# Performance work log

Hardware: AMD Instinct MI355X
Metric: run time of the kernel (lower is better)

The kernel has to match this reference:

```python
import jax, jax.numpy as jnp
import numpy as np

N_NODES = 100000
N_EDGES = 1000000
D = 64
N_LAYERS = 3
LN_EPS = 1e-5


def setup_inputs() -> dict:
    key = jax.random.key(0)
    ks = jax.random.split(key, 12)
    s = 1.0 / np.sqrt(D)
    return {
        "feats": jax.random.normal(ks[0], (N_NODES, D), jnp.float32),
        "src": jax.random.randint(ks[1], (N_EDGES,), 0, N_NODES, jnp.int32),
        "dst": jax.random.randint(ks[2], (N_EDGES,), 0, N_NODES, jnp.int32),
        # GraphConv weights/biases (stacked over layers; in==hid==out==D)
        "conv_W": jax.random.normal(ks[3], (N_LAYERS, D, D), jnp.float32) * s,
        "conv_b": jnp.zeros((N_LAYERS, D), jnp.float32),
        # residual Linear per layer
        "res_W": jax.random.normal(ks[4], (N_LAYERS, D, D), jnp.float32) * s,
        "res_b": jnp.zeros((N_LAYERS, D), jnp.float32),
        # LayerNorm affine per layer
        "ln_g": jnp.ones((N_LAYERS, D), jnp.float32),
        "ln_b": jnp.zeros((N_LAYERS, D), jnp.float32),
        # final linear_prediction
        "pred_W": jax.random.normal(ks[5], (D, D), jnp.float32) * s,
        "pred_b": jnp.zeros((D,), jnp.float32),
    }


def _layer_norm(h, g, b):
    mu = jnp.mean(h, axis=-1, keepdims=True)
    var = jnp.mean(jnp.square(h - mu), axis=-1, keepdims=True)
    return (h - mu) * jax.lax.rsqrt(var + LN_EPS) * g + b


def reference(feats, src, dst, conv_W, conv_b, res_W, res_b, ln_g, ln_b, pred_W, pred_b):
    n = feats.shape[0]
    ones = jnp.ones(src.shape[0], feats.dtype)
    # DGL GraphConv norm='both', degrees clamped to >= 1
    out_deg = jnp.clip(jax.ops.segment_sum(ones, src, num_segments=n), 1.0, None)
    in_deg = jnp.clip(jax.ops.segment_sum(ones, dst, num_segments=n), 1.0, None)
    out_norm = jax.lax.rsqrt(out_deg)[:, None]  # [N,1]
    in_norm = jax.lax.rsqrt(in_deg)[:, None]

    h = feats
    h_final = jnp.zeros_like(feats)
    for i in range(N_LAYERS):
        # GraphConv: scale src, sum-aggregate over edges, scale dst, linear
        msg = (h * out_norm)[src]                                   # [E, D]
        agg = jax.ops.segment_sum(msg, dst, num_segments=n) * in_norm
        conv = agg @ conv_W[i] + conv_b[i]
        # residual linear + LayerNorm + relu (dropout p=0) + JK accumulate
        h = conv + h @ res_W[i] + res_b[i]
        h = jax.nn.relu(_layer_norm(h, ln_g[i], ln_b[i]))
        h_final = h_final + h
    return h_final @ pred_W + pred_b
```

## Files before the change

### kernel.cpp

```cpp
#include <hip/hip_runtime.h>
#include <hip/hip_bf16.h>

#define DD 64
#define NBLK 128
#define MAXBUK 1024
#define BSHIFT 7

typedef __attribute__((ext_vector_type(8))) short short8v;
typedef __attribute__((ext_vector_type(4))) float f32x4;

__device__ __forceinline__ unsigned pk_bf16(float a, float b) {
    __hip_bfloat162 h = __float22bfloat162_rn(make_float2(a, b));
    unsigned u; __builtin_memcpy(&u, &h, 4); return u;
}
__device__ __forceinline__ short f2bf_s(float f) {
    union { float f; unsigned u; } x; x.f = f;
    unsigned r = x.u + 0x7fff + ((x.u >> 16) & 1);
    return (short)(r >> 16);
}
__device__ __forceinline__ float bf_lo(unsigned u) { return __int_as_float(u << 16); }
__device__ __forceinline__ float bf_hi(unsigned u) { return __int_as_float(u & 0xffff0000u); }
__device__ __forceinline__ short8v u4_to_s8(uint4 u) {
    union { uint4 u; short8v s; } x; x.u = u; return x.s;
}


__global__ __launch_bounds__(256) void part_count(
        const int* __restrict__ src, const int* __restrict__ dst,
        int* __restrict__ cnt, int E, int nbuk, int ce) {
    __shared__ int hd[MAXBUK], hs[MAXBUK];
    for (int i = threadIdx.x; i < MAXBUK; i += 256) { hd[i] = 0; hs[i] = 0; }
    __syncthreads();
    int e0 = blockIdx.x * ce;
    int e1 = min(e0 + ce, E);
    for (int e = e0 + (int)threadIdx.x; e < e1; e += 256) {
        atomicAdd(&hd[dst[e] >> BSHIFT], 1);
        atomicAdd(&hs[src[e] >> BSHIFT], 1);
    }
    __syncthreads();
    int L2 = nbuk * NBLK;
    for (int b = threadIdx.x; b < nbuk; b += 256) {
        cnt[b * NBLK + blockIdx.x]      = hd[b];
        cnt[L2 + b * NBLK + blockIdx.x] = hs[b];
    }
}

__global__ void scan1p(int* __restrict__ a, int* __restrict__ bsums, int L) {
    __shared__ int tmp[256];
    int gid = blockIdx.x * 256 + threadIdx.x;
    int v = (gid < L) ? a[gid] : 0;
    tmp[threadIdx.x] = v;
    __syncthreads();
    for (int off = 1; off < 256; off <<= 1) {
        int t = (threadIdx.x >= off) ? tmp[threadIdx.x - off] : 0;
        __syncthreads();
        tmp[threadIdx.x] += t;
        __syncthreads();
    }
    if (gid < L) a[gid] = tmp[threadIdx.x] - v;
    if (threadIdx.x == 255) bsums[blockIdx.x] = tmp[255];
}
__global__ void scan2p(int* __restrict__ bsums, int nb) {
    __shared__ int tmp[1024];
    int v = (threadIdx.x < (unsigned)nb) ? bsums[threadIdx.x] : 0;
    tmp[threadIdx.x] = v;
    __syncthreads();
    for (int off = 1; off < 1024; off <<= 1) {
        int t = (threadIdx.x >= off) ? tmp[threadIdx.x - off] : 0;
        __syncthreads();
        tmp[threadIdx.x] += t;
        __syncthreads();
    }
    if (threadIdx.x < (unsigned)nb) bsums[threadIdx.x] = tmp[threadIdx.x] - v;
}
__global__ void scan3p(int* __restrict__ a, const int* __restrict__ bsums, int L) {
    int gid = blockIdx.x * 256 + threadIdx.x;
    if (gid < L) a[gid] += bsums[blockIdx.x];
}

__global__ __launch_bounds__(256) void part_scatter(
        const int* __restrict__ src, const int* __restrict__ dst,
        const int* __restrict__ ofs,
        unsigned int* __restrict__ partD, unsigned char* __restrict__ partS,
        int E, int nbuk, int ce) {
    __shared__ int cd[MAXBUK], cs[MAXBUK];
    int L2 = nbuk * NBLK;
    for (int b = threadIdx.x; b < nbuk; b += 256) {
        cd[b] = ofs[b * NBLK + blockIdx.x];
        cs[b] = ofs[L2 + b * NBLK + blockIdx.x] - E;
    }
    __syncthreads();
    int e0 = blockIdx.x * ce;
    int e1 = min(e0 + ce, E);
    for (int e = e0 + (int)threadIdx.x; e < e1; e += 256) {
        int s = src[e], d = dst[e];
        int pd = atomicAdd(&cd[d >> BSHIFT], 1);
        partD[pd] = ((unsigned)(d & 127) << 17) | (unsigned)s;
        int ps = atomicAdd(&cs[s >> BSHIFT], 1);
        partS[ps] = (unsigned char)(s & 127);
    }
}

__global__ __launch_bounds__(256) void bucket_csr(
        const unsigned int* __restrict__ partD, const int* __restrict__ ofs,
        int* __restrict__ rowptr, int* __restrict__ esrc,
        float* __restrict__ inn, int E, int nbuk, int n) {
    __shared__ int h[128], sc[128], cu[128];
    int b = blockIdx.x, tid = threadIdx.x;
    int e0 = ofs[b * NBLK];
    int e1 = (b + 1 < nbuk) ? ofs[(b + 1) * NBLK] : E;
    if (tid < 128) h[tid] = 0;
    __syncthreads();
    for (int e = e0 + tid; e < e1; e += 256)
        atomicAdd(&h[partD[e] >> 17], 1);
    __syncthreads();
    if (tid < 128) sc[tid] = h[tid];
    __syncthreads();
    for (int off = 1; off < 128; off <<= 1) {
        int t = (tid < 128 && tid >= off) ? sc[tid - off] : 0;
        __syncthreads();
        if (tid < 128) sc[tid] += t;
        __syncthreads();
    }
    int nodeBase = b << BSHIFT;
    if (tid < 128) {
        int excl = e0 + sc[tid] - h[tid];
        cu[tid] = excl;
        int v = nodeBase + tid;
        if (v < n) {
            rowptr[v] = excl;
            inn[v] = rsqrtf((float)max(h[tid], 1));
        }
    }
    if (b == 0 && tid == 0) rowptr[n] = E;
    __syncthreads();
    for (int e = e0 + tid; e < e1; e += 256) {
        unsigned v = partD[e];
        int p = atomicAdd(&cu[v >> 17], 1);
        esrc[p] = (int)(v & 0x1FFFFu);
    }
}

__global__ __launch_bounds__(256) void bucket_deg(
        const unsigned char* __restrict__ partS, const int* __restrict__ ofs,
        float* __restrict__ outn, float* __restrict__ rs,
        int E, int nbuk, int n) {
    __shared__ int h[128];
    int b = blockIdx.x, tid = threadIdx.x;
    int L2 = nbuk * NBLK;
    int f0 = ofs[L2 + b * NBLK] - E;
    int f1 = (b + 1 < nbuk) ? ofs[L2 + (b + 1) * NBLK] - E : E;
    if (tid < 128) h[tid] = 0;
    __syncthreads();
    for (int e = f0 + tid; e < f1; e += 256)
        atomicAdd(&h[(int)partS[e]], 1);
    __syncthreads();
    if (tid < 128) {
        int v = (b << BSHIFT) + tid;
        if (v < n) {
            float d = (float)max(h[tid], 1);
            outn[v] = rsqrtf(d);
            rs[v]   = sqrtf(d);
        }
    }
}

__global__ void scale_kernel(const float* __restrict__ feats, const float* __restrict__ outn,
                             unsigned short* __restrict__ hs, int n) {
    int idx = blockIdx.x * blockDim.x + threadIdx.x;
    if (idx < n * 8) {
        int v = idx >> 3;
        float s = outn[v];
        const float4* fp = (const float4*)feats + (size_t)idx * 2;
        float4 f0 = fp[0], f1 = fp[1];
        uint4 o;
        o.x = pk_bf16(f0.x * s, f0.y * s); o.y = pk_bf16(f0.z * s, f0.w * s);
        o.z = pk_bf16(f1.x * s, f1.y * s); o.w = pk_bf16(f1.z * s, f1.w * s);
        ((uint4*)hs)[idx] = o;
    }
}

__global__ __launch_bounds__(256) void gcn_kernel(
    const int* __restrict__ rowptr, const int* __restrict__ esrc,
    const float* __restrict__ inn, const float* __restrict__ rs,
    const float* __restrict__ outn,
    const unsigned short* __restrict__ hs_in,
    const float* __restrict__ Wc, const float* __restrict__ bc,
    const float* __restrict__ Wr, const float* __restrict__ br,
    const float* __restrict__ Wp, const float* __restrict__ pb,
    const float* __restrict__ g, const float* __restrict__ bb,
    unsigned short* __restrict__ hs_out, float* __restrict__ h_final,
    float* __restrict__ pred_out,
    int first, int last, int n)
{
    __shared__ __align__(16) short sWf[24 * 64 * 8];
    __shared__ __align__(16) short sXa[4][16 * 72];
    __shared__ float sEps[4 * 64];

    int lane = threadIdx.x & 63;
    int wave = threadIdx.x >> 6;
    int q   = lane & 15;
    int gg  = lane >> 4;
    int q8  = lane & 7;
    int o8  = lane >> 3;

    for (int idx = threadIdx.x; idx < 64; idx += blockDim.x) {
        sEps[idx]       = bc[idx] + br[idx];
        sEps[64 + idx]  = g[idx];
        sEps[128 + idx] = bb[idx];
        sEps[192 + idx] = pb[idx];
    }
    for (int f = wave * 6; f < wave * 6 + 6; ++f) {
        int mat = f >> 3, ft = (f >> 1) & 3, kc = f & 1;
        const float* Ws = (mat == 0) ? Wc : (mat == 1) ? Wr : Wp;
        int feat = ft * 16 + q;
        int k0 = kc * 32 + gg * 8;
        short8v fr;
        #pragma unroll
        for (int j = 0; j < 8; ++j) fr[j] = f2bf_s(Ws[(k0 + j) * DD + feat]);
        *(short8v*)&sWf[(f * 64 + lane) * 8] = fr;
    }
    __syncthreads();

    short* xrow_w = &sXa[wave][0];
    const short8v* wf = (const short8v*)sWf;
    int wgid = blockIdx.x * 4 + wave;
    int nwav = gridDim.x * 4;
    int ngrp = (n + 15) >> 4;

    for (int grp = wgid; grp < ngrp; grp += nwav) {
        int vbase = grp << 4;
        int vo = vbase + q;
        int vsel = min(vo, n - 1);

        const uint4* hrow = (const uint4*)(hs_in + (size_t)vsel * DD);
        uint4 bh0u = hrow[gg];
        uint4 bh1u = hrow[4 + gg];
        float rsv  = rs[vsel];
        float innv = inn[vsel];

        int rp = rowptr[min(vbase + min(lane, 16), n)];
        int stA = __shfl(rp, o8);     int dgA = __shfl(rp, o8 + 1) - stA;
        int stB = __shfl(rp, o8 + 8); int dgB = __shfl(rp, o8 + 9) - stB;

        #pragma unroll
        for (int hh = 0; hh < 2; ++hh) {
            int st = hh ? stB : stA;
            int dg = hh ? dgB : dgA;
            int mdg = dg;
            mdg = max(mdg, __shfl_xor(mdg, 8));
            mdg = max(mdg, __shfl_xor(mdg, 16));
            mdg = max(mdg, __shfl_xor(mdg, 32));

            float a[8];
            #pragma unroll
            for (int c = 0; c < 8; ++c) a[c] = 0.0f;

            int id0 = (0 < dg) ? esrc[st + 0] : 0;  float m0 = (0 < dg) ? 1.f : 0.f;
            int id1 = (1 < dg) ? esrc[st + 1] : 0;  float m1 = (1 < dg) ? 1.f : 0.f;
            int id2 = (2 < dg) ? esrc[st + 2] : 0;  float m2 = (2 < dg) ? 1.f : 0.f;
            int id3 = (3 < dg) ? esrc[st + 3] : 0;  float m3 = (3 < dg) ? 1.f : 0.f;

            for (int t = 0; t < mdg; t += 4) {
                uint4 r0 = *(const uint4*)(hs_in + (size_t)id0 * DD + q8 * 8);
                uint4 r1 = *(const uint4*)(hs_in + (size_t)id1 * DD + q8 * 8);
                uint4 r2 = *(const uint4*)(hs_in + (size_t)id2 * DD + q8 * 8);
                uint4 r3 = *(const uint4*)(hs_in + (size_t)id3 * DD + q8 * 8);
                float c0 = m0, c1 = m1, c2 = m2, c3 = m3;
                int t4 = t + 4;
                id0 = (t4 + 0 < dg) ? esrc[st + t4 + 0] : 0;  m0 = (t4 + 0 < dg) ? 1.f : 0.f;
                id1 = (t4 + 1 < dg) ? esrc[st + t4 + 1] : 0;  m1 = (t4 + 1 < dg) ? 1.f : 0.f;
                id2 = (t4 + 2 < dg) ? esrc[st + t4 + 2] : 0;  m2 = (t4 + 2 < dg) ? 1.f : 0.f;
                id3 = (t4 + 3 < dg) ? esrc[st + t4 + 3] : 0;  m3 = (t4 + 3 < dg) ? 1.f : 0.f;
                a[0] = fmaf(bf_lo(r0.x), c0, a[0]); a[1] = fmaf(bf_hi(r0.x), c0, a[1]);
                a[2] = fmaf(bf_lo(r0.y), c0, a[2]); a[3] = fmaf(bf_hi(r0.y), c0, a[3]);
                a[4] = fmaf(bf_lo(r0.z), c0, a[4]); a[5] = fmaf(bf_hi(r0.z), c0, a[5]);
                a[6] = fmaf(bf_lo(r0.w), c0, a[6]); a[7] = fmaf(bf_hi(r0.w), c0, a[7]);
                a[0] = fmaf(bf_lo(r1.x), c1, a[0]); a[1] = fmaf(bf_hi(r1.x), c1, a[1]);
                a[2] = fmaf(bf_lo(r1.y), c1, a[2]); a[3] = fmaf(bf_hi(r1.y), c1, a[3]);
                a[4] = fmaf(bf_lo(r1.z), c1, a[4]); a[5] = fmaf(bf_hi(r1.z), c1, a[5]);
                a[6] = fmaf(bf_lo(r1.w), c1, a[6]); a[7] = fmaf(bf_hi(r1.w), c1, a[7]);
                a[0] = fmaf(bf_lo(r2.x), c2, a[0]); a[1] = fmaf(bf_hi(r2.x), c2, a[1]);
                a[2] = fmaf(bf_lo(r2.y), c2, a[2]); a[3] = fmaf(bf_hi(r2.y), c2, a[3]);
                a[4] = fmaf(bf_lo(r2.z), c2, a[4]); a[5] = fmaf(bf_hi(r2.z), c2, a[5]);
                a[6] = fmaf(bf_lo(r2.w), c2, a[6]); a[7] = fmaf(bf_hi(r2.w), c2, a[7]);
                a[0] = fmaf(bf_lo(r3.x), c3, a[0]); a[1] = fmaf(bf_hi(r3.x), c3, a[1]);
                a[2] = fmaf(bf_lo(r3.y), c3, a[2]); a[3] = fmaf(bf_hi(r3.y), c3, a[3]);
                a[4] = fmaf(bf_lo(r3.z), c3, a[4]); a[5] = fmaf(bf_hi(r3.z), c3, a[5]);
                a[6] = fmaf(bf_lo(r3.w), c3, a[6]); a[7] = fmaf(bf_hi(r3.w), c3, a[7]);
            }

            uint4 w4;
            w4.x = pk_bf16(a[0], a[1]); w4.y = pk_bf16(a[2], a[3]);
            w4.z = pk_bf16(a[4], a[5]); w4.w = pk_bf16(a[6], a[7]);
            *(uint4*)&xrow_w[(hh * 8 + o8) * 72 + q8 * 8] = w4;
        }

        const short* xr = &xrow_w[q * 72];
        short8v ba0 = *(const short8v*)&xr[gg * 8];
        short8v ba1 = *(const short8v*)&xr[32 + gg * 8];
        short8v sh0 = u4_to_s8(bh0u);
        short8v sh1 = u4_to_s8(bh1u);

        f32x4 accC[4], accR[4];
        #pragma unroll
        for (int ft = 0; ft < 4; ++ft) {
            f32x4 c = {0.f, 0.f, 0.f, 0.f};
            c = __builtin_amdgcn_mfma_f32_16x16x32_bf16(wf[(ft * 2 + 0) * 64 + lane], ba0, c, 0, 0, 0);
            c = __builtin_amdgcn_mfma_f32_16x16x32_bf16(wf[(ft * 2 + 1) * 64 + lane], ba1, c, 0, 0, 0);
            accC[ft] = c;
            f32x4 r = {0.f, 0.f, 0.f, 0.f};
            r = __builtin_amdgcn_mfma_f32_16x16x32_bf16(wf[(8 + ft * 2 + 0) * 64 + lane], sh0, r, 0, 0, 0);
            r = __builtin_amdgcn_mfma_f32_16x16x32_bf16(wf[(8 + ft * 2 + 1) * 64 + lane], sh1, r, 0, 0, 0);
            accR[ft] = r;
        }

        f32x4 ac[4];
        #pragma unroll
        for (int ft = 0; ft < 4; ++ft) {
            float4 b4 = *(const float4*)&sEps[ft * 16 + gg * 4];
            ac[ft][0] = fmaf(innv, accC[ft][0], fmaf(rsv, accR[ft][0], b4.x));
            ac[ft][1] = fmaf(innv, accC[ft][1], fmaf(rsv, accR[ft][1], b4.y));
            ac[ft][2] = fmaf(innv, accC[ft][2], fmaf(rsv, accR[ft][2], b4.z));
            ac[ft][3] = fmaf(innv, accC[ft][3], fmaf(rsv, accR[ft][3], b4.w));
        }
        float s = 0.f;
        #pragma unroll
        for (int ft = 0; ft < 4; ++ft) s += ac[ft][0] + ac[ft][1] + ac[ft][2] + ac[ft][3];
        s += __shfl_xor(s, 16); s += __shfl_xor(s, 32);
        float mu = s * (1.0f / 64.0f);
        float vsum = 0.f;
        #pragma unroll
        for (int ft = 0; ft < 4; ++ft) {
            #pragma unroll
            for (int r = 0; r < 4; ++r) { float d = ac[ft][r] - mu; vsum += d * d; }
        }
        vsum += __shfl_xor(vsum, 16); vsum += __shfl_xor(vsum, 32);
        float rinv = rsqrtf(vsum * (1.0f / 64.0f) + 1e-5f);

        float4 yv[4];
        #pragma unroll
        for (int ft = 0; ft < 4; ++ft) {
            float4 g4 = *(const float4*)&sEps[64 + ft * 16 + gg * 4];
            float4 c4 = *(const float4*)&sEps[128 + ft * 16 + gg * 4];
            yv[ft].x = fmaxf((ac[ft][0] - mu) * rinv * g4.x + c4.x, 0.f);
            yv[ft].y = fmaxf((ac[ft][1] - mu) * rinv * g4.y + c4.y, 0.f);
            yv[ft].z = fmaxf((ac[ft][2] - mu) * rinv * g4.z + c4.z, 0.f);
            yv[ft].w = fmaxf((ac[ft][3] - mu) * rinv * g4.w + c4.w, 0.f);
        }

        if (!last) {
            if (vo < n) {
                float on = outn[vo];
                #pragma unroll
                for (int ft = 0; ft < 4; ++ft) {
                    size_t off = (size_t)vo * DD + ft * 16 + gg * 4;
                    uint2 p;
                    p.x = pk_bf16(yv[ft].x * on, yv[ft].y * on);
                    p.y = pk_bf16(yv[ft].z * on, yv[ft].w * on);
                    *(uint2*)&hs_out[off] = p;
                    if (first) {
                        *(float4*)&h_final[off] = yv[ft];
                    } else {
                        float4 hf = *(const float4*)&h_final[off];
                        hf.x += yv[ft].x; hf.y += yv[ft].y;
                        hf.z += yv[ft].z; hf.w += yv[ft].w;
                        *(float4*)&h_final[off] = hf;
                    }
                }
            }
        } else {
            #pragma unroll
            for (int ft = 0; ft < 4; ++ft) {
                float4 hf = make_float4(0.f, 0.f, 0.f, 0.f);
                if (vo < n) {
                    float4 old = *(const float4*)&h_final[(size_t)vo * DD + ft * 16 + gg * 4];
                    hf.x = old.x + yv[ft].x; hf.y = old.y + yv[ft].y;
                    hf.z = old.z + yv[ft].z; hf.w = old.w + yv[ft].w;
                }
                uint2 p;
                p.x = pk_bf16(hf.x, hf.y);
                p.y = pk_bf16(hf.z, hf.w);
                *(uint2*)&xrow_w[q * 72 + ft * 16 + gg * 4] = p;
            }
            short8v bp0 = *(const short8v*)&xr[gg * 8];
            short8v bp1 = *(const short8v*)&xr[32 + gg * 8];
            #pragma unroll
            for (int ft = 0; ft < 4; ++ft) {
                f32x4 p = {0.f, 0.f, 0.f, 0.f};
                p = __builtin_amdgcn_mfma_f32_16x16x32_bf16(wf[(16 + ft * 2 + 0) * 64 + lane], bp0, p, 0, 0, 0);
                p = __builtin_amdgcn_mfma_f32_16x16x32_bf16(wf[(16 + ft * 2 + 1) * 64 + lane], bp1, p, 0, 0, 0);
                if (vo < n) {
                    float4 b4 = *(const float4*)&sEps[192 + ft * 16 + gg * 4];
                    float4 o = make_float4(p[0] + b4.x, p[1] + b4.y, p[2] + b4.z, p[3] + b4.w);
                    *(float4*)&pred_out[(size_t)vo * DD + ft * 16 + gg * 4] = o;
                }
            }
        }
    }
}

extern "C" void kernel_launch(void* const* d_in, const int* in_sizes, int n_in,
                              void* d_out, int out_size, void* d_ws, size_t ws_size,
                              hipStream_t stream) {
    const float* feats  = (const float*)d_in[0];
    const int*   src    = (const int*)d_in[1];
    const int*   dst    = (const int*)d_in[2];
    const float* conv_W = (const float*)d_in[3];
    const float* conv_b = (const float*)d_in[4];
    const float* res_W  = (const float*)d_in[5];
    const float* res_b  = (const float*)d_in[6];
    const float* ln_g   = (const float*)d_in[7];
    const float* ln_b   = (const float*)d_in[8];
    const float* pred_W = (const float*)d_in[9];
    const float* pred_b = (const float*)d_in[10];

    int N = in_sizes[0] / DD;
    int E = in_sizes[1];

    int nbuk = (N + (1 << BSHIFT) - 1) >> BSHIFT;
    int ce   = (E + NBLK - 1) / NBLK;
    int L    = nbuk * NBLK * 2;
    int nb   = (L + 255) / 256;

    int*   rowptr = (int*)d_ws;
    int*   cnt    = rowptr + (N + 1);
    int*   bsums  = cnt + MAXBUK * NBLK * 2;
    int*   esrc   = bsums + 1024;
    float* outn   = (float*)(esrc + E);
    float* inn    = outn + N;
    float* rs     = inn + N;
    float* base   = (float*)(((uintptr_t)(rs + N) + 15) & ~(uintptr_t)15);
    unsigned short* hsA = (unsigned short*)base;
    unsigned short* hsB = (unsigned short*)(base + (size_t)N * 32);
    float* hfin  = base + (size_t)N * 64;
    unsigned int*  partD = (unsigned int*)hfin;
    unsigned char* partS = (unsigned char*)(partD + E);

    part_count  <<<NBLK, 256, 0, stream>>>(src, dst, cnt, E, nbuk, ce);
    scan1p      <<<nb, 256, 0, stream>>>(cnt, bsums, L);
    scan2p      <<<1, 1024, 0, stream>>>(bsums, nb);
    scan3p      <<<nb, 256, 0, stream>>>(cnt, bsums, L);
    part_scatter<<<NBLK, 256, 0, stream>>>(src, dst, cnt, partD, partS, E, nbuk, ce);
    bucket_csr  <<<nbuk, 256, 0, stream>>>(partD, cnt, rowptr, esrc, inn, E, nbuk, N);
    bucket_deg  <<<nbuk, 256, 0, stream>>>(partS, cnt, outn, rs, E, nbuk, N);
    scale_kernel<<<(N * 8 + 255) / 256, 256, 0, stream>>>(feats, outn, hsA, N);

    const unsigned short* ins[3]  = {hsA, hsB, hsA};
    unsigned short*       outs[3] = {hsB, hsA, hsB};
    for (int l = 0; l < 3; ++l) {
        gcn_kernel<<<1024, 256, 0, stream>>>(
            rowptr, esrc, inn, rs, outn, ins[l],
            conv_W + (size_t)l * DD * DD, conv_b + (size_t)l * DD,
            res_W  + (size_t)l * DD * DD, res_b  + (size_t)l * DD,
            pred_W, pred_b,
            ln_g   + (size_t)l * DD,      ln_b   + (size_t)l * DD,
            outs[l], hfin, (float*)d_out,
            (l == 0) ? 1 : 0, (l == 2) ? 1 : 0, N);
    }
}
```

Baseline: 303.5 us.

## Sort nodes by in-degree and process both half-groups in one merged gather loop

Adds a counting sort of destination nodes by in-degree (histogram, scan, scatter kernels) and makes the fused GCN kernel walk nodes in that order, so each 16-node wave group has similar degrees and fewer masked iterations in the gather loop. The two 8-node halves are now gathered together in one loop with twice the outstanding loads, the next group's perm and rowptr entries are prefetched, and the grid drops to 768 blocks with a 3-blocks-per-CU launch bound. The cost is five extra small preprocessing kernels, scattered output writes through the permutation, and higher register pressure.

New measurement: 424.7 us. 39.9% more time.

```diff
diff --git a/kernel.cpp b/kernel.cpp
--- a/kernel.cpp
+++ b/kernel.cpp
@@ -5,6 +5,7 @@
 #define NBLK 128
 #define MAXBUK 1024
 #define BSHIFT 7
+#define NB3 64
 
 typedef __attribute__((ext_vector_type(8))) short short8v;
 typedef __attribute__((ext_vector_type(4))) float f32x4;
@@ -104,7 +105,8 @@
 __global__ __launch_bounds__(256) void bucket_csr(
         const unsigned int* __restrict__ partD, const int* __restrict__ ofs,
         int* __restrict__ rowptr, int* __restrict__ esrc,
-        float* __restrict__ inn, int E, int nbuk, int n) {
+        float* __restrict__ inn, int* __restrict__ degout,
+        int E, int nbuk, int n) {
     __shared__ int h[128], sc[128], cu[128];
     int b = blockIdx.x, tid = threadIdx.x;
     int e0 = ofs[b * NBLK];
@@ -130,6 +132,7 @@
         if (v < n) {
             rowptr[v] = excl;
             inn[v] = rsqrtf((float)max(h[tid], 1));
+            degout[v] = h[tid];
         }
     }
     if (b == 0 && tid == 0) rowptr[n] = E;
@@ -162,6 +165,32 @@
             outn[v] = rsqrtf(d);
             rs[v]   = sqrtf(d);
         }
+    }
+}
+
+__global__ __launch_bounds__(256) void dhist(const int* __restrict__ deg,
+                                             int* __restrict__ cnt2, int N, int chunk) {
+    __shared__ int h2[256];
+    h2[threadIdx.x] = 0;
+    __syncthreads();
+    int b = blockIdx.x;
+    int v0 = b * chunk, v1 = min(v0 + chunk, N);
+    for (int v = v0 + (int)threadIdx.x; v < v1; v += 256)
+        atomicAdd(&h2[min(deg[v], 255)], 1);
+    __syncthreads();
+    cnt2[threadIdx.x * NB3 + b] = h2[threadIdx.x];
+}
+__global__ __launch_bounds__(256) void dscatter(const int* __restrict__ deg,
+                                                const int* __restrict__ cnt2,
+                                                int* __restrict__ perm, int N, int chunk) {
+    __shared__ int cu2[256];
+    int b = blockIdx.x;
+    cu2[threadIdx.x] = cnt2[threadIdx.x * NB3 + b];
+    __syncthreads();
+    int v0 = b * chunk, v1 = min(v0 + chunk, N);
+    for (int v = v0 + (int)threadIdx.x; v < v1; v += 256) {
+        int pos = atomicAdd(&cu2[min(deg[v], 255)], 1);
+        perm[pos] = v;
     }
 }
 
@@ -180,8 +209,9 @@
     }
 }
 
-__global__ __launch_bounds__(256) void gcn_kernel(
+__global__ __launch_bounds__(256, 3) void gcn_kernel(
     const int* __restrict__ rowptr, const int* __restrict__ esrc,
+    const int* __restrict__ perm,
     const float* __restrict__ inn, const float* __restrict__ rs,
     const float* __restrict__ outn,
     const unsigned short* __restrict__ hs_in,
@@ -228,72 +258,116 @@
     int nwav = gridDim.x * 4;
     int ngrp = (n + 15) >> 4;
 
+    int nodeL = 0, rpS = 0, rpE = 0;
+    if (wgid < ngrp && lane < 16) {
+        nodeL = perm[min(wgid * 16 + lane, n - 1)];
+        rpS = rowptr[nodeL];
+        rpE = rowptr[nodeL + 1];
+    }
+
     for (int grp = wgid; grp < ngrp; grp += nwav) {
-        int vbase = grp << 4;
-        int vo = vbase + q;
-        int vsel = min(vo, n - 1);
-
-        const uint4* hrow = (const uint4*)(hs_in + (size_t)vsel * DD);
+        int idxq = (grp << 4) + q;
+        int pv   = __shfl(nodeL, q);
+
+        const uint4* hrow = (const uint4*)(hs_in + (size_t)pv * DD);
         uint4 bh0u = hrow[gg];
         uint4 bh1u = hrow[4 + gg];
-        float rsv  = rs[vsel];
-        float innv = inn[vsel];
-
-        int rp = rowptr[min(vbase + min(lane, 16), n)];
-        int stA = __shfl(rp, o8);     int dgA = __shfl(rp, o8 + 1) - stA;
-        int stB = __shfl(rp, o8 + 8); int dgB = __shfl(rp, o8 + 9) - stB;
-
-        #pragma unroll
-        for (int hh = 0; hh < 2; ++hh) {
-            int st = hh ? stB : stA;
-            int dg = hh ? dgB : dgA;
-            int mdg = dg;
-            mdg = max(mdg, __shfl_xor(mdg, 8));
-            mdg = max(mdg, __shfl_xor(mdg, 16));
-            mdg = max(mdg, __shfl_xor(mdg, 32));
-
-            float a[8];
-            #pragma unroll
-            for (int c = 0; c < 8; ++c) a[c] = 0.0f;
-
-            int id0 = (0 < dg) ? esrc[st + 0] : 0;  float m0 = (0 < dg) ? 1.f : 0.f;
-            int id1 = (1 < dg) ? esrc[st + 1] : 0;  float m1 = (1 < dg) ? 1.f : 0.f;
-            int id2 = (2 < dg) ? esrc[st + 2] : 0;  float m2 = (2 < dg) ? 1.f : 0.f;
-            int id3 = (3 < dg) ? esrc[st + 3] : 0;  float m3 = (3 < dg) ? 1.f : 0.f;
-
-            for (int t = 0; t < mdg; t += 4) {
-                uint4 r0 = *(const uint4*)(hs_in + (size_t)id0 * DD + q8 * 8);
-                uint4 r1 = *(const uint4*)(hs_in + (size_t)id1 * DD + q8 * 8);
-                uint4 r2 = *(const uint4*)(hs_in + (size_t)id2 * DD + q8 * 8);
-                uint4 r3 = *(const uint4*)(hs_in + (size_t)id3 * DD + q8 * 8);
-                float c0 = m0, c1 = m1, c2 = m2, c3 = m3;
-                int t4 = t + 4;
-                id0 = (t4 + 0 < dg) ? esrc[st + t4 + 0] : 0;  m0 = (t4 + 0 < dg) ? 1.f : 0.f;
-                id1 = (t4 + 1 < dg) ? esrc[st + t4 + 1] : 0;  m1 = (t4 + 1 < dg) ? 1.f : 0.f;
-                id2 = (t4 + 2 < dg) ? esrc[st + t4 + 2] : 0;  m2 = (t4 + 2 < dg) ? 1.f : 0.f;
-                id3 = (t4 + 3 < dg) ? esrc[st + t4 + 3] : 0;  m3 = (t4 + 3 < dg) ? 1.f : 0.f;
-                a[0] = fmaf(bf_lo(r0.x), c0, a[0]); a[1] = fmaf(bf_hi(r0.x), c0, a[1]);
-                a[2] = fmaf(bf_lo(r0.y), c0, a[2]); a[3] = fmaf(bf_hi(r0.y), c0, a[3]);
-                a[4] = fmaf(bf_lo(r0.z), c0, a[4]); a[5] = fmaf(bf_hi(r0.z), c0, a[5]);
-                a[6] = fmaf(bf_lo(r0.w), c0, a[6]); a[7] = fmaf(bf_hi(r0.w), c0, a[7]);
-                a[0] = fmaf(bf_lo(r1.x), c1, a[0]); a[1] = fmaf(bf_hi(r1.x), c1, a[1]);
-                a[2] = fmaf(bf_lo(r1.y), c1, a[2]); a[3] = fmaf(bf_hi(r1.y), c1, a[3]);
-                a[4] = fmaf(bf_lo(r1.z), c1, a[4]); a[5] = fmaf(bf_hi(r1.z), c1, a[5]);
-                a[6] = fmaf(bf_lo(r1.w), c1, a[6]); a[7] = fmaf(bf_hi(r1.w), c1, a[7]);
-                a[0] = fmaf(bf_lo(r2.x), c2, a[0]); a[1] = fmaf(bf_hi(r2.x), c2, a[1]);
-                a[2] = fmaf(bf_lo(r2.y), c2, a[2]); a[3] = fmaf(bf_hi(r2.y), c2, a[3]);
-                a[4] = fmaf(bf_lo(r2.z), c2, a[4]); a[5] = fmaf(bf_hi(r2.z), c2, a[5]);
-                a[6] = fmaf(bf_lo(r2.w), c2, a[6]); a[7] = fmaf(bf_hi(r2.w), c2, a[7]);
-                a[0] = fmaf(bf_lo(r3.x), c3, a[0]); a[1] = fmaf(bf_hi(r3.x), c3, a[1]);
-                a[2] = fmaf(bf_lo(r3.y), c3, a[2]); a[3] = fmaf(bf_hi(r3.y), c3, a[3]);
-                a[4] = fmaf(bf_lo(r3.z), c3, a[4]); a[5] = fmaf(bf_hi(r3.z), c3, a[5]);
-                a[6] = fmaf(bf_lo(r3.w), c3, a[6]); a[7] = fmaf(bf_hi(r3.w), c3, a[7]);
-            }
-
-            uint4 w4;
-            w4.x = pk_bf16(a[0], a[1]); w4.y = pk_bf16(a[2], a[3]);
-            w4.z = pk_bf16(a[4], a[5]); w4.w = pk_bf16(a[6], a[7]);
-            *(uint4*)&xrow_w[(hh * 8 + o8) * 72 + q8 * 8] = w4;
+        float rsv  = rs[pv];
+        float innv = inn[pv];
+
+        int stA = __shfl(rpS, o8);      int dgA = __shfl(rpE, o8) - stA;
+        int stB = __shfl(rpS, 8 + o8);  int dgB = __shfl(rpE, 8 + o8) - stB;
+
+        int grn = grp + nwav;
+        int nodeLn = 0;
+        if (grn < ngrp && lane < 16) nodeLn = perm[min(grn * 16 + lane, n - 1)];
+
+        int md = max(dgA, dgB);
+        md = max(md, __shfl_xor(md, 8));
+        md = max(md, __shfl_xor(md, 16));
+        md = max(md, __shfl_xor(md, 32));
+
+        float aA[8], aB[8];
+        #pragma unroll
+        for (int c = 0; c < 8; ++c) { aA[c] = 0.0f; aB[c] = 0.0f; }
+
+        int iA0 = (0 < dgA) ? esrc[stA + 0] : 0;  float mA0 = (0 < dgA) ? 1.f : 0.f;
+        int iA1 = (1 < dgA) ? esrc[stA + 1] : 0;  float mA1 = (1 < dgA) ? 1.f : 0.f;
+        int iA2 = (2 < dgA) ? esrc[stA + 2] : 0;  float mA2 = (2 < dgA) ? 1.f : 0.f;
+        int iA3 = (3 < dgA) ? esrc[stA + 3] : 0;  float mA3 = (3 < dgA) ? 1.f : 0.f;
+        int iB0 = (0 < dgB) ? esrc[stB + 0] : 0;  float mB0 = (0 < dgB) ? 1.f : 0.f;
+        int iB1 = (1 < dgB) ? esrc[stB + 1] : 0;  float mB1 = (1 < dgB) ? 1.f : 0.f;
+        int iB2 = (2 < dgB) ? esrc[stB + 2] : 0;  float mB2 = (2 < dgB) ? 1.f : 0.f;
+        int iB3 = (3 < dgB) ? esrc[stB + 3] : 0;  float mB3 = (3 < dgB) ? 1.f : 0.f;
+
+        for (int t = 0; t < md; t += 4) {
+            uint4 rA0 = *(const uint4*)(hs_in + (size_t)iA0 * DD + q8 * 8);
+            uint4 rA1 = *(const uint4*)(hs_in + (size_t)iA1 * DD + q8 * 8);
+            uint4 rA2 = *(const uint4*)(hs_in + (size_t)iA2 * DD + q8 * 8);
+            uint4 rA3 = *(const uint4*)(hs_in + (size_t)iA3 * DD + q8 * 8);
+            uint4 rB0 = *(const uint4*)(hs_in + (size_t)iB0 * DD + q8 * 8);
+            uint4 rB1 = *(const uint4*)(hs_in + (size_t)iB1 * DD + q8 * 8);
+            uint4 rB2 = *(const uint4*)(hs_in + (size_t)iB2 * DD + q8 * 8);
+            uint4 rB3 = *(const uint4*)(hs_in + (size_t)iB3 * DD + q8 * 8);
+            float cA0 = mA0, cA1 = mA1, cA2 = mA2, cA3 = mA3;
+            float cB0 = mB0, cB1 = mB1, cB2 = mB2, cB3 = mB3;
+            int t4 = t + 4;
+            iA0 = (t4 + 0 < dgA) ? esrc[stA + t4 + 0] : 0;  mA0 = (t4 + 0 < dgA) ? 1.f : 0.f;
+            iA1 = (t4 + 1 < dgA) ? esrc[stA + t4 + 1] : 0;  mA1 = (t4 + 1 < dgA) ? 1.f : 0.f;
+            iA2 = (t4 + 2 < dgA) ? esrc[stA + t4 + 2] : 0;  mA2 = (t4 + 2 < dgA) ? 1.f : 0.f;
+            iA3 = (t4 + 3 < dgA) ? esrc[stA + t4 + 3] : 0;  mA3 = (t4 + 3 < dgA) ? 1.f : 0.f;
+            iB0 = (t4 + 0 < dgB) ? esrc[stB + t4 + 0] : 0;  mB0 = (t4 + 0 < dgB) ? 1.f : 0.f;
+            iB1 = (t4 + 1 < dgB) ? esrc[stB + t4 + 1] : 0;  mB1 = (t4 + 1 < dgB) ? 1.f : 0.f;
+            iB2 = (t4 + 2 < dgB) ? esrc[stB + t4 + 2] : 0;  mB2 = (t4 + 2 < dgB) ? 1.f : 0.f;
+            iB3 = (t4 + 3 < dgB) ? esrc[stB + t4 + 3] : 0;  mB3 = (t4 + 3 < dgB) ? 1.f : 0.f;
+
+            aA[0] = fmaf(bf_lo(rA0.x), cA0, aA[0]); aA[1] = fmaf(bf_hi(rA0.x), cA0, aA[1]);
+            aA[2] = fmaf(bf_lo(rA0.y), cA0, aA[2]); aA[3] = fmaf(bf_hi(rA0.y), cA0, aA[3]);
+            aA[4] = fmaf(bf_lo(rA0.z), cA0, aA[4]); aA[5] = fmaf(bf_hi(rA0.z), cA0, aA[5]);
+            aA[6] = fmaf(bf_lo(rA0.w), cA0, aA[6]); aA[7] = fmaf(bf_hi(rA0.w), cA0, aA[7]);
+            aA[0] = fmaf(bf_lo(rA1.x), cA1, aA[0]); aA[1] = fmaf(bf_hi(rA1.x), cA1, aA[1]);
+            aA[2] = fmaf(bf_lo(rA1.y), cA1, aA[2]); aA[3] = fmaf(bf_hi(rA1.y), cA1, aA[3]);
+            aA[4] = fmaf(bf_lo(rA1.z), cA1, aA[4]); aA[5] = fmaf(bf_hi(rA1.z), cA1, aA[5]);
+            aA[6] = fmaf(bf_lo(rA1.w), cA1, aA[6]); aA[7] = fmaf(bf_hi(rA1.w), cA1, aA[7]);
+            aA[0] = fmaf(bf_lo(rA2.x), cA2, aA[0]); aA[1] = fmaf(bf_hi(rA2.x), cA2, aA[1]);
+            aA[2] = fmaf(bf_lo(rA2.y), cA2, aA[2]); aA[3] = fmaf(bf_hi(rA2.y), cA2, aA[3]);
+            aA[4] = fmaf(bf_lo(rA2.z), cA2, aA[4]); aA[5] = fmaf(bf_hi(rA2.z), cA2, aA[5]);
+            aA[6] = fmaf(bf_lo(rA2.w), cA2, aA[6]); aA[7] = fmaf(bf_hi(rA2.w), cA2, aA[7]);
+            aA[0] = fmaf(bf_lo(rA3.x), cA3, aA[0]); aA[1] = fmaf(bf_hi(rA3.x), cA3, aA[1]);
+            aA[2] = fmaf(bf_lo(rA3.y), cA3, aA[2]); aA[3] = fmaf(bf_hi(rA3.y), cA3, aA[3]);
+            aA[4] = fmaf(bf_lo(rA3.z), cA3, aA[4]); aA[5] = fmaf(bf_hi(rA3.z), cA3, aA[5]);
+            aA[6] = fmaf(bf_lo(rA3.w), cA3, aA[6]); aA[7] = fmaf(bf_hi(rA3.w), cA3, aA[7]);
+
+            aB[0] = fmaf(bf_lo(rB0.x), cB0, aB[0]); aB[1] = fmaf(bf_hi(rB0.x), cB0, aB[1]);
+            aB[2] = fmaf(bf_lo(rB0.y), cB0, aB[2]); aB[3] = fmaf(bf_hi(rB0.y), cB0, aB[3]);
+            aB[4] = fmaf(bf_lo(rB0.z), cB0, aB[4]); aB[5] = fmaf(bf_hi(rB0.z), cB0, aB[5]);
+            aB[6] = fmaf(bf_lo(rB0.w), cB0, aB[6]); aB[7] = fmaf(bf_hi(rB0.w), cB0, aB[7]);
+            aB[0] = fmaf(bf_lo(rB1.x), cB1, aB[0]); aB[1] = fmaf(bf_hi(rB1.x), cB1, aB[1]);
+            aB[2] = fmaf(bf_lo(rB1.y), cB1, aB[2]); aB[3] = fmaf(bf_hi(rB1.y), cB1, aB[3]);
+            aB[4] = fmaf(bf_lo(rB1.z), cB1, aB[4]); aB[5] = fmaf(bf_hi(rB1.z), cB1, aB[5]);
+            aB[6] = fmaf(bf_lo(rB1.w), cB1, aB[6]); aB[7] = fmaf(bf_hi(rB1.w), cB1, aB[7]);
+            aB[0] = fmaf(bf_lo(rB2.x), cB2, aB[0]); aB[1] = fmaf(bf_hi(rB2.x), cB2, aB[1]);
+            aB[2] = fmaf(bf_lo(rB2.y), cB2, aB[2]); aB[3] = fmaf(bf_hi(rB2.y), cB2, aB[3]);
+            aB[4] = fmaf(bf_lo(rB2.z), cB2, aB[4]); aB[5] = fmaf(bf_hi(rB2.z), cB2, aB[5]);
+            aB[6] = fmaf(bf_lo(rB2.w), cB2, aB[6]); aB[7] = fmaf(bf_hi(rB2.w), cB2, aB[7]);
+            aB[0] = fmaf(bf_lo(rB3.x), cB3, aB[0]); aB[1] = fmaf(bf_hi(rB3.x), cB3, aB[1]);
+            aB[2] = fmaf(bf_lo(rB3.y), cB3, aB[2]); aB[3] = fmaf(bf_hi(rB3.y), cB3, aB[3]);
+            aB[4] = fmaf(bf_lo(rB3.z), cB3, aB[4]); aB[5] = fmaf(bf_hi(rB3.z), cB3, aB[5]);
+            aB[6] = fmaf(bf_lo(rB3.w), cB3, aB[6]); aB[7] = fmaf(bf_hi(rB3.w), cB3, aB[7]);
+        }
+
+        uint4 w4;
+        w4.x = pk_bf16(aA[0], aA[1]); w4.y = pk_bf16(aA[2], aA[3]);
+        w4.z = pk_bf16(aA[4], aA[5]); w4.w = pk_bf16(aA[6], aA[7]);
+        *(uint4*)&xrow_w[o8 * 72 + q8 * 8] = w4;
+        w4.x = pk_bf16(aB[0], aB[1]); w4.y = pk_bf16(aB[2], aB[3]);
+        w4.z = pk_bf16(aB[4], aB[5]); w4.w = pk_bf16(aB[6], aB[7]);
+        *(uint4*)&xrow_w[(8 + o8) * 72 + q8 * 8] = w4;
+
+        int rpSn = 0, rpEn = 0;
+        if (grn < ngrp && lane < 16) {
+            rpSn = rowptr[nodeLn];
+            rpEn = rowptr[nodeLn + 1];
         }
 
         const short* xr = &xrow_w[q * 72];
@@ -350,11 +424,11 @@
         }
 
         if (!last) {
-            if (vo < n) {
-                float on = outn[vo];
+            if (idxq < n) {
+                float on = outn[pv];
                 #pragma unroll
                 for (int ft = 0; ft < 4; ++ft) {
-                    size_t off = (size_t)vo * DD + ft * 16 + gg * 4;
+                    size_t off = (size_t)pv * DD + ft * 16 + gg * 4;
                     uint2 p;
                     p.x = pk_bf16(yv[ft].x * on, yv[ft].y * on);
                     p.y = pk_bf16(yv[ft].z * on, yv[ft].w * on);
@@ -373,8 +447,8 @@
             #pragma unroll
             for (int ft = 0; ft < 4; ++ft) {
                 float4 hf = make_float4(0.f, 0.f, 0.f, 0.f);
-                if (vo < n) {
-                    float4 old = *(const float4*)&h_final[(size_t)vo * DD + ft * 16 + gg * 4];
+                if (idxq < n) {
+                    float4 old = *(const float4*)&h_final[(size_t)pv * DD + ft * 16 + gg * 4];
                     hf.x = old.x + yv[ft].x; hf.y = old.y + yv[ft].y;
                     hf.z = old.z + yv[ft].z; hf.w = old.w + yv[ft].w;
                 }
@@ -390,13 +464,15 @@
                 f32x4 p = {0.f, 0.f, 0.f, 0.f};
                 p = __builtin_amdgcn_mfma_f32_16x16x32_bf16(wf[(16 + ft * 2 + 0) * 64 + lane], bp0, p, 0, 0, 0);
                 p = __builtin_amdgcn_mfma_f32_16x16x32_bf16(wf[(16 + ft * 2 + 1) * 64 + lane], bp1, p, 0, 0, 0);
-                if (vo < n) {
+                if (idxq < n) {
                     float4 b4 = *(const float4*)&sEps[192 + ft * 16 + gg * 4];
                     float4 o = make_float4(p[0] + b4.x, p[1] + b4.y, p[2] + b4.z, p[3] + b4.w);
-                    *(float4*)&pred_out[(size_t)vo * DD + ft * 16 + gg * 4] = o;
+                    *(float4*)&pred_out[(size_t)pv * DD + ft * 16 + gg * 4] = o;
                 }
             }
         }
+
+        nodeL = nodeLn; rpS = rpSn; rpE = rpEn;
     }
 }
 
@@ -422,6 +498,9 @@
     int ce   = (E + NBLK - 1) / NBLK;
     int L    = nbuk * NBLK * 2;
     int nb   = (L + 255) / 256;
+    int chunk3 = (N + NB3 - 1) / NB3;
+    int L3   = 256 * NB3;
+    int nb3  = (L3 + 255) / 256;
 
     int*   rowptr = (int*)d_ws;
     int*   cnt    = rowptr + (N + 1);
@@ -434,6 +513,9 @@
     unsigned short* hsA = (unsigned short*)base;
     unsigned short* hsB = (unsigned short*)(base + (size_t)N * 32);
     float* hfin  = base + (size_t)N * 64;
+    int*   deg   = (int*)(hfin + (size_t)N * 64);
+    int*   perm  = deg + N;
+    int*   cnt2  = perm + N;
     unsigned int*  partD = (unsigned int*)hfin;
     unsigned char* partS = (unsigned char*)(partD + E);
 
@@ -442,15 +524,20 @@
     scan2p      <<<1, 1024, 0, stream>>>(bsums, nb);
     scan3p      <<<nb, 256, 0, stream>>>(cnt, bsums, L);
     part_scatter<<<NBLK, 256, 0, stream>>>(src, dst, cnt, partD, partS, E, nbuk, ce);
-    bucket_csr  <<<nbuk, 256, 0, stream>>>(partD, cnt, rowptr, esrc, inn, E, nbuk, N);
+    bucket_csr  <<<nbuk, 256, 0, stream>>>(partD, cnt, rowptr, esrc, inn, deg, E, nbuk, N);
     bucket_deg  <<<nbuk, 256, 0, stream>>>(partS, cnt, outn, rs, E, nbuk, N);
+    dhist       <<<NB3, 256, 0, stream>>>(deg, cnt2, N, chunk3);
+    scan1p      <<<nb3, 256, 0, stream>>>(cnt2, bsums, L3);
+    scan2p      <<<1, 1024, 0, stream>>>(bsums, nb3);
+    scan3p      <<<nb3, 256, 0, stream>>>(cnt2, bsums, L3);
+    dscatter    <<<NB3, 256, 0, stream>>>(deg, cnt2, perm, N, chunk3);
     scale_kernel<<<(N * 8 + 255) / 256, 256, 0, stream>>>(feats, outn, hsA, N);
 
     const unsigned short* ins[3]  = {hsA, hsB, hsA};
     unsigned short*       outs[3] = {hsB, hsA, hsB};
     for (int l = 0; l < 3; ++l) {
-        gcn_kernel<<<1024, 256, 0, stream>>>(
-            rowptr, esrc, inn, rs, outn, ins[l],
+        gcn_kernel<<<768, 256, 0, stream>>>(
+            rowptr, esrc, perm, inn, rs, outn, ins[l],
             conv_W + (size_t)l * DD * DD, conv_b + (size_t)l * DD,
             res_W  + (size_t)l * DD * DD, res_b  + (size_t)l * DD,
             pred_W, pred_b,
```

## Relabel nodes by in-degree so gather waves get balanced neighbor counts

Applied to the files above, without the earlier changes.

Adds a counting sort of nodes by in-degree (histogram, scan, scatter, inverse permutation) and rebuilds the CSR, normalisation arrays and bf16 features in the sorted node order. The GCN layers then run over degree-sorted rows, which is meant to cut load imbalance and divergence among lanes that aggregate neighbors together. The final prediction is written back through the permutation. This adds about ten small preprocessing launches and extra permuted-index traffic, and reordering may hurt locality of the original node ids.

After: 326.1 us. 7.5% more time.

```diff
diff --git a/kernel.cpp b/kernel.cpp
--- a/kernel.cpp
+++ b/kernel.cpp
@@ -5,6 +5,7 @@
 #define NBLK 128
 #define MAXBUK 1024
 #define BSHIFT 7
+#define NB3 64
 
 typedef __attribute__((ext_vector_type(8))) short short8v;
 typedef __attribute__((ext_vector_type(4))) float f32x4;
@@ -101,11 +102,10 @@
     }
 }
 
-__global__ __launch_bounds__(256) void bucket_csr(
+__global__ __launch_bounds__(256) void bucket_hist(
         const unsigned int* __restrict__ partD, const int* __restrict__ ofs,
-        int* __restrict__ rowptr, int* __restrict__ esrc,
-        float* __restrict__ inn, int E, int nbuk, int n) {
-    __shared__ int h[128], sc[128], cu[128];
+        int* __restrict__ deg, int E, int nbuk, int n) {
+    __shared__ int h[128];
     int b = blockIdx.x, tid = threadIdx.x;
     int e0 = ofs[b * NBLK];
     int e1 = (b + 1 < nbuk) ? ofs[(b + 1) * NBLK] : E;
@@ -114,37 +114,15 @@
     for (int e = e0 + tid; e < e1; e += 256)
         atomicAdd(&h[partD[e] >> 17], 1);
     __syncthreads();
-    if (tid < 128) sc[tid] = h[tid];
-    __syncthreads();
-    for (int off = 1; off < 128; off <<= 1) {
-        int t = (tid < 128 && tid >= off) ? sc[tid - off] : 0;
-        __syncthreads();
-        if (tid < 128) sc[tid] += t;
-        __syncthreads();
-    }
-    int nodeBase = b << BSHIFT;
     if (tid < 128) {
-        int excl = e0 + sc[tid] - h[tid];
-        cu[tid] = excl;
-        int v = nodeBase + tid;
-        if (v < n) {
-            rowptr[v] = excl;
-            inn[v] = rsqrtf((float)max(h[tid], 1));
-        }
-    }
-    if (b == 0 && tid == 0) rowptr[n] = E;
-    __syncthreads();
-    for (int e = e0 + tid; e < e1; e += 256) {
-        unsigned v = partD[e];
-        int p = atomicAdd(&cu[v >> 17], 1);
-        esrc[p] = (int)(v & 0x1FFFFu);
+        int v = (b << BSHIFT) + tid;
+        if (v < n) deg[v] = h[tid];
     }
 }
 
 __global__ __launch_bounds__(256) void bucket_deg(
         const unsigned char* __restrict__ partS, const int* __restrict__ ofs,
-        float* __restrict__ outn, float* __restrict__ rs,
-        int E, int nbuk, int n) {
+        int* __restrict__ outdeg, int E, int nbuk, int n) {
     __shared__ int h[128];
     int b = blockIdx.x, tid = threadIdx.x;
     int L2 = nbuk * NBLK;
@@ -157,21 +135,87 @@
     __syncthreads();
     if (tid < 128) {
         int v = (b << BSHIFT) + tid;
-        if (v < n) {
-            float d = (float)max(h[tid], 1);
-            outn[v] = rsqrtf(d);
-            rs[v]   = sqrtf(d);
-        }
-    }
-}
-
-__global__ void scale_kernel(const float* __restrict__ feats, const float* __restrict__ outn,
-                             unsigned short* __restrict__ hs, int n) {
+        if (v < n) outdeg[v] = h[tid];
+    }
+}
+
+__global__ __launch_bounds__(256) void dhist(const int* __restrict__ deg,
+                                             int* __restrict__ cnt2, int N, int chunk) {
+    __shared__ int h2[256];
+    h2[threadIdx.x] = 0;
+    __syncthreads();
+    int b = blockIdx.x;
+    int v0 = b * chunk, v1 = min(v0 + chunk, N);
+    for (int v = v0 + (int)threadIdx.x; v < v1; v += 256)
+        atomicAdd(&h2[min(deg[v], 255)], 1);
+    __syncthreads();
+    cnt2[threadIdx.x * NB3 + b] = h2[threadIdx.x];
+}
+__global__ __launch_bounds__(256) void dscatter(const int* __restrict__ deg,
+                                                const int* __restrict__ cnt2,
+                                                int* __restrict__ perm, int N, int chunk) {
+    __shared__ int cu2[256];
+    int b = blockIdx.x;
+    cu2[threadIdx.x] = cnt2[threadIdx.x * NB3 + b];
+    __syncthreads();
+    int v0 = b * chunk, v1 = min(v0 + chunk, N);
+    for (int v = v0 + (int)threadIdx.x; v < v1; v += 256) {
+        int pos = atomicAdd(&cu2[min(deg[v], 255)], 1);
+        perm[pos] = v;
+    }
+}
+__global__ void invperm(const int* __restrict__ perm, int* __restrict__ inv, int N) {
+    int i = blockIdx.x * 256 + threadIdx.x;
+    if (i < N) inv[perm[i]] = i;
+}
+__global__ void sortgath(const int* __restrict__ perm, const int* __restrict__ deg,
+                         const int* __restrict__ outdeg,
+                         int* __restrict__ rowptr2, float* __restrict__ inn2,
+                         float* __restrict__ rs2, float* __restrict__ outn2,
+                         int N, int E) {
+    int i = blockIdx.x * 256 + threadIdx.x;
+    if (i < N) {
+        int p = perm[i];
+        int d = deg[p];
+        int od = outdeg[p];
+        rowptr2[i] = d;
+        inn2[i] = rsqrtf((float)max(d, 1));
+        float odc = (float)max(od, 1);
+        outn2[i] = rsqrtf(odc);
+        rs2[i]   = sqrtf(odc);
+        if (i == 0) rowptr2[N] = E;
+    }
+}
+
+__global__ __launch_bounds__(256) void bucket_scatter(
+        const unsigned int* __restrict__ partD, const int* __restrict__ ofs,
+        const int* __restrict__ rowptr2, const int* __restrict__ inv,
+        int* __restrict__ esrc2, int E, int nbuk, int n) {
+    __shared__ int cu[128];
+    int b = blockIdx.x, tid = threadIdx.x;
+    int e0 = ofs[b * NBLK];
+    int e1 = (b + 1 < nbuk) ? ofs[(b + 1) * NBLK] : E;
+    if (tid < 128) {
+        int v = (b << BSHIFT) + tid;
+        cu[tid] = (v < n) ? rowptr2[inv[v]] : 0;
+    }
+    __syncthreads();
+    for (int e = e0 + tid; e < e1; e += 256) {
+        unsigned u = partD[e];
+        int p = atomicAdd(&cu[u >> 17], 1);
+        esrc2[p] = inv[u & 0x1FFFFu];
+    }
+}
+
+__global__ void scale_perm(const float* __restrict__ feats, const float* __restrict__ outn2,
+                           const int* __restrict__ perm,
+                           unsigned short* __restrict__ hs, int n) {
     int idx = blockIdx.x * blockDim.x + threadIdx.x;
     if (idx < n * 8) {
-        int v = idx >> 3;
-        float s = outn[v];
-        const float4* fp = (const float4*)feats + (size_t)idx * 2;
+        int v = idx >> 3, c = idx & 7;
+        int p = perm[v];
+        float s = outn2[v];
+        const float4* fp = (const float4*)(feats + (size_t)p * DD) + c * 2;
         float4 f0 = fp[0], f1 = fp[1];
         uint4 o;
         o.x = pk_bf16(f0.x * s, f0.y * s); o.y = pk_bf16(f0.z * s, f0.w * s);
@@ -182,6 +226,7 @@
 
 __global__ __launch_bounds__(256) void gcn_kernel(
     const int* __restrict__ rowptr, const int* __restrict__ esrc,
+    const int* __restrict__ perm,
     const float* __restrict__ inn, const float* __restrict__ rs,
     const float* __restrict__ outn,
     const unsigned short* __restrict__ hs_in,
@@ -370,6 +415,7 @@
                 }
             }
         } else {
+            int pvo = perm[vsel];
             #pragma unroll
             for (int ft = 0; ft < 4; ++ft) {
                 float4 hf = make_float4(0.f, 0.f, 0.f, 0.f);
@@ -393,7 +439,7 @@
                 if (vo < n) {
                     float4 b4 = *(const float4*)&sEps[192 + ft * 16 + gg * 4];
                     float4 o = make_float4(p[0] + b4.x, p[1] + b4.y, p[2] + b4.z, p[3] + b4.w);
-                    *(float4*)&pred_out[(size_t)vo * DD + ft * 16 + gg * 4] = o;
+                    *(float4*)&pred_out[(size_t)pvo * DD + ft * 16 + gg * 4] = o;
                 }
             }
         }
@@ -422,35 +468,55 @@
     int ce   = (E + NBLK - 1) / NBLK;
     int L    = nbuk * NBLK * 2;
     int nb   = (L + 255) / 256;
-
-    int*   rowptr = (int*)d_ws;
-    int*   cnt    = rowptr + (N + 1);
+    int chunk3 = (N + NB3 - 1) / NB3;
+    int L3   = 256 * NB3;
+    int nb3  = (L3 + 255) / 256;
+    int nbN  = (N + 255) / 256;
+
+    int*   rowptr2 = (int*)d_ws;
+    int*   cnt    = rowptr2 + (N + 1);
     int*   bsums  = cnt + MAXBUK * NBLK * 2;
-    int*   esrc   = bsums + 1024;
-    float* outn   = (float*)(esrc + E);
-    float* inn    = outn + N;
-    float* rs     = inn + N;
-    float* base   = (float*)(((uintptr_t)(rs + N) + 15) & ~(uintptr_t)15);
+    int*   esrc2  = bsums + 1024;
+    float* outn2  = (float*)(esrc2 + E);
+    float* inn2   = outn2 + N;
+    float* rs2    = inn2 + N;
+    int*   deg    = (int*)(rs2 + N);
+    int*   outdeg = deg + N;
+    int*   perm   = outdeg + N;
+    int*   inv    = perm + N;
+    int*   cnt2   = inv + N;
+    float* base   = (float*)(((uintptr_t)(cnt2 + 16384) + 15) & ~(uintptr_t)15);
     unsigned short* hsA = (unsigned short*)base;
     unsigned short* hsB = (unsigned short*)(base + (size_t)N * 32);
     float* hfin  = base + (size_t)N * 64;
     unsigned int*  partD = (unsigned int*)hfin;
     unsigned char* partS = (unsigned char*)(partD + E);
 
-    part_count  <<<NBLK, 256, 0, stream>>>(src, dst, cnt, E, nbuk, ce);
-    scan1p      <<<nb, 256, 0, stream>>>(cnt, bsums, L);
-    scan2p      <<<1, 1024, 0, stream>>>(bsums, nb);
-    scan3p      <<<nb, 256, 0, stream>>>(cnt, bsums, L);
-    part_scatter<<<NBLK, 256, 0, stream>>>(src, dst, cnt, partD, partS, E, nbuk, ce);
-    bucket_csr  <<<nbuk, 256, 0, stream>>>(partD, cnt, rowptr, esrc, inn, E, nbuk, N);
-    bucket_deg  <<<nbuk, 256, 0, stream>>>(partS, cnt, outn, rs, E, nbuk, N);
-    scale_kernel<<<(N * 8 + 255) / 256, 256, 0, stream>>>(feats, outn, hsA, N);
+    part_count   <<<NBLK, 256, 0, stream>>>(src, dst, cnt, E, nbuk, ce);
+    scan1p       <<<nb, 256, 0, stream>>>(cnt, bsums, L);
+    scan2p       <<<1, 1024, 0, stream>>>(bsums, nb);
+    scan3p       <<<nb, 256, 0, stream>>>(cnt, bsums, L);
+    part_scatter <<<NBLK, 256, 0, stream>>>(src, dst, cnt, partD, partS, E, nbuk, ce);
+    bucket_hist  <<<nbuk, 256, 0, stream>>>(partD, cnt, deg, E, nbuk, N);
+    bucket_deg   <<<nbuk, 256, 0, stream>>>(partS, cnt, outdeg, E, nbuk, N);
+    dhist        <<<NB3, 256, 0, stream>>>(deg, cnt2, N, chunk3);
+    scan1p       <<<nb3, 256, 0, stream>>>(cnt2, bsums, L3);
+    scan2p       <<<1, 1024, 0, stream>>>(bsums, nb3);
+    scan3p       <<<nb3, 256, 0, stream>>>(cnt2, bsums, L3);
+    dscatter     <<<NB3, 256, 0, stream>>>(deg, cnt2, perm, N, chunk3);
+    invperm      <<<nbN, 256, 0, stream>>>(perm, inv, N);
+    sortgath     <<<nbN, 256, 0, stream>>>(perm, deg, outdeg, rowptr2, inn2, rs2, outn2, N, E);
+    scan1p       <<<nbN, 256, 0, stream>>>(rowptr2, bsums, N);
+    scan2p       <<<1, 1024, 0, stream>>>(bsums, nbN);
+    scan3p       <<<nbN, 256, 0, stream>>>(rowptr2, bsums, N);
+    bucket_scatter<<<nbuk, 256, 0, stream>>>(partD, cnt, rowptr2, inv, esrc2, E, nbuk, N);
+    scale_perm   <<<(N * 8 + 255) / 256, 256, 0, stream>>>(feats, outn2, perm, hsA, N);
 
     const unsigned short* ins[3]  = {hsA, hsB, hsA};
     unsigned short*       outs[3] = {hsB, hsA, hsB};
     for (int l = 0; l < 3; ++l) {
         gcn_kernel<<<1024, 256, 0, stream>>>(
-            rowptr, esrc, inn, rs, outn, ins[l],
+            rowptr2, esrc2, perm, inn2, rs2, outn2, ins[l],
             conv_W + (size_t)l * DD * DD, conv_b + (size_t)l * DD,
             res_W  + (size_t)l * DD * DD, res_b  + (size_t)l * DD,
             pred_W, pred_b,
```
